# Kernel tuning notes

Hardware: AMD Instinct MI355X
Metric: run time of the kernel (lower is better)

The kernel has to match this reference:

```python
import jax, jax.numpy as jnp
import numpy as np

DECAY = 0.99
EPS = 1e-05


def setup_inputs() -> dict:
    key = jax.random.key(0)
    k1, k2, k3, k4 = jax.random.split(key, 4)
    x = jax.random.normal(k1, (32, 64, 64, 64), jnp.float32)          # [B,H,W,dim]
    embed = jax.random.normal(k2, (64, 1024), jnp.float32)            # [dim, n_embed] buffer
    cluster_size = jax.random.uniform(k3, (1024,), jnp.float32)       # EMA cluster-size buffer
    embed_avg = jax.random.normal(k4, (64, 1024), jnp.float32)        # EMA embed-avg buffer
    return {"x": x, "embed": embed, "cluster_size": cluster_size, "embed_avg": embed_avg}


def reference(x, embed, cluster_size, embed_avg):
    dim = x.shape[-1]
    n_embed = embed.shape[1]
    flatten = x.reshape(-1, dim)                                      # [N, dim]
    # squared distances: ||f||^2 - 2 f.E + ||e||^2   -> [N, n_embed]
    dist = ((flatten * flatten).sum(1, keepdims=True)
            - 2.0 * (flatten @ embed)
            + (embed * embed).sum(0, keepdims=True))
    idx = jnp.argmin(dist, axis=1)                                    # [N]
    quantize = jnp.take(embed.T, idx, axis=0).reshape(x.shape)        # codebook gather
    embed_ind = idx.reshape(x.shape[:-1])

    # EMA codebook update (training branch); stats detached as in torch (buffers, .data ops)
    fl = jax.lax.stop_gradient(flatten)
    onehot_sum = jax.ops.segment_sum(jnp.ones_like(idx, dtype=x.dtype), idx, num_segments=n_embed)
    embed_sum = jax.ops.segment_sum(fl, idx, num_segments=n_embed).T  # [dim, n_embed]
    new_cluster_size = DECAY * cluster_size + (1.0 - DECAY) * onehot_sum
    new_embed_avg = DECAY * embed_avg + (1.0 - DECAY) * embed_sum
    n = new_cluster_size.sum()
    cs = (new_cluster_size + EPS) / (n + n_embed * EPS) * n
    new_embed = new_embed_avg / cs[None, :]

    diff = jnp.mean((jax.lax.stop_gradient(quantize) - x) ** 2)       # commitment loss
    quantize_st = x + jax.lax.stop_gradient(quantize - x)             # straight-through
    return (quantize_st, diff, embed_ind, new_cluster_size, new_embed_avg, new_embed)
```

## Files before the change

### kernel.cpp

```cpp
#include <hip/hip_runtime.h>


#define N_ROWS 131072
#define DIM    64
#define NEMB   1024
#define FLAG_CAP 131072
#define TAU 0.02f
#define NRANGE 32

static constexpr float DECAYF = 0.99f;
static constexpr float OMDF   = (float)(1.0 - 0.99);
static constexpr float EPSF   = 1e-5f;
static constexpr float NEPSF  = (float)(1024 * 1e-5);

typedef __attribute__((ext_vector_type(8))) short short8;
typedef __attribute__((ext_vector_type(4))) float f32x4;

static __device__ __forceinline__ unsigned short f2bf(float f) {
    unsigned int u = __builtin_bit_cast(unsigned int, f);
    unsigned int r = (u + 0x7FFFu + ((u >> 16) & 1u)) >> 16;
    return (unsigned short)r;
}
static __device__ __forceinline__ float bf2f(unsigned short h) {
    unsigned int u = ((unsigned int)h) << 16;
    return __builtin_bit_cast(float, u);
}

#define WS_ESUM    0
#define WS_CNTF    65536
#define WS_DIFF    66560
#define WS_FLAGCNT 66561
#define WS_N       66562
#define WS_EE      66564
#define WS_EMBEDT  67588
#define WS_IDX     133124
#define WS_FLAGLST 264196
#define WS_BFRAG   395268
#define WS_CNTPART 460804
#define WS_PART    493572
#define WS_NEED_BYTES ((size_t)(WS_PART + NRANGE * 65536) * 4)

__global__ void prep_kernel(const float* __restrict__ embed,
                            float* __restrict__ embedT,
                            float* __restrict__ ee,
                            uint4* __restrict__ BfragG) {
    int tid = blockIdx.x * 256 + threadIdx.x;
    for (int i = 0; i < 4; ++i) {
        int id = i * 16384 + tid;
        int d = id >> 10, e = id & 1023;
        embedT[e * 64 + d] = embed[id];
    }
    if (tid < NEMB) {
        float s = 0.f;
        for (int d = 0; d < DIM; ++d) {
            float v = embed[d * 1024 + tid];
            s = fmaf(v, v, s);
        }
        ee[tid] = s;
    }
    int fid  = tid >> 6;
    int lane = tid & 63;
    int hl = fid & 1, kt = (fid >> 1) & 1, ct = fid >> 2;
    int col = ct * 16 + (lane & 15);
    int k0  = kt * 32 + (lane >> 4) * 8;
    unsigned short u[8];
    #pragma unroll
    for (int j = 0; j < 8; ++j) {
        float v = -2.0f * embed[(k0 + j) * 1024 + col];
        unsigned short h = f2bf(v);
        if (hl) h = f2bf(v - bf2f(h));
        u[j] = h;
    }
    uint4 wv;
    wv.x = (unsigned)u[0] | ((unsigned)u[1] << 16);
    wv.y = (unsigned)u[2] | ((unsigned)u[3] << 16);
    wv.z = (unsigned)u[4] | ((unsigned)u[5] << 16);
    wv.w = (unsigned)u[6] | ((unsigned)u[7] << 16);
    BfragG[fid * 64 + lane] = wv;
}

__global__ __launch_bounds__(256) void dist_kernel(
        const float* __restrict__ x, const uint4* __restrict__ BfragG,
        const float* __restrict__ ee, const float* __restrict__ embedT,
        float* __restrict__ out_q, float* __restrict__ out_ind,
        int* __restrict__ ws_idx, float* __restrict__ ws_diff,
        int* __restrict__ ws_flagcnt, int* __restrict__ ws_flaglist) {
    __shared__ float sEE[1024];
    __shared__ int   sIdx[128];
    __shared__ float red[4];

    const int t = threadIdx.x;
    const int w = t >> 6, lane = t & 63;
    const int quad = lane >> 4, wl = lane & 15;
    const int rbase = blockIdx.x * 128;

    short8 a_hi[2][2], a_lo[2][2];
    #pragma unroll
    for (int rt = 0; rt < 2; ++rt) {
        int row = rbase + w * 32 + rt * 16 + wl;
        #pragma unroll
        for (int kt = 0; kt < 2; ++kt) {
            const float* px = x + (size_t)row * 64 + kt * 32 + quad * 8;
            float4 v0 = *(const float4*)px;
            float4 v1 = *(const float4*)(px + 4);
            float vv[8] = {v0.x, v0.y, v0.z, v0.w, v1.x, v1.y, v1.z, v1.w};
            short8 ah, al;
            #pragma unroll
            for (int j = 0; j < 8; ++j) {
                unsigned short h = f2bf(vv[j]);
                ah[j] = (short)h;
                al[j] = (short)f2bf(vv[j] - bf2f(h));
            }
            a_hi[rt][kt] = ah; a_lo[rt][kt] = al;
        }
    }

    for (int i = t; i < 1024; i += 256) sEE[i] = ee[i];

    float b1[8], b2[8];
    int   i1[8];
    #pragma unroll
    for (int s = 0; s < 8; ++s) { b1[s] = 3.4e38f; b2[s] = 3.4e38f; i1[s] = 0; }

    const f32x4 zacc = {0.f, 0.f, 0.f, 0.f};

    __syncthreads();

    const uint4* bg = BfragG + lane;
    uint4 nb0 = bg[0], nb1 = bg[64], nb2 = bg[128], nb3 = bg[192];
    for (int g = 0; g < 64; ++g) {
        uint4 c_b0 = nb0, c_b1 = nb1, c_b2 = nb2, c_b3 = nb3;
        if (g < 63) {
            const uint4* p = bg + (g + 1) * 256;
            nb0 = p[0]; nb1 = p[64]; nb2 = p[128]; nb3 = p[192];
        }
        short8 bh0 = __builtin_bit_cast(short8, c_b0);
        short8 bl0 = __builtin_bit_cast(short8, c_b1);
        short8 bh1 = __builtin_bit_cast(short8, c_b2);
        short8 bl1 = __builtin_bit_cast(short8, c_b3);
        int col = g * 16 + wl;
        float eec = sEE[col];
        #pragma unroll
        for (int rt = 0; rt < 2; ++rt) {
            f32x4 c0 = __builtin_amdgcn_mfma_f32_16x16x32_bf16(a_lo[rt][0], bh0, zacc, 0, 0, 0);
            f32x4 c1 = __builtin_amdgcn_mfma_f32_16x16x32_bf16(a_lo[rt][1], bh1, zacc, 0, 0, 0);
            c0 = __builtin_amdgcn_mfma_f32_16x16x32_bf16(a_hi[rt][0], bl0, c0, 0, 0, 0);
            c1 = __builtin_amdgcn_mfma_f32_16x16x32_bf16(a_hi[rt][1], bl1, c1, 0, 0, 0);
            c0 = __builtin_amdgcn_mfma_f32_16x16x32_bf16(a_hi[rt][0], bh0, c0, 0, 0, 0);
            c1 = __builtin_amdgcn_mfma_f32_16x16x32_bf16(a_hi[rt][1], bh1, c1, 0, 0, 0);
            #pragma unroll
            for (int reg = 0; reg < 4; ++reg) {
                float s = c0[reg] + c1[reg] + eec;
                int st = rt * 4 + reg;
                bool lt = s < b1[st];
                b2[st] = fminf(fmaxf(s, b1[st]), b2[st]);
                i1[st] = lt ? col : i1[st];
                b1[st] = fminf(s, b1[st]);
            }
        }
    }

    for (int m = 1; m < 16; m <<= 1) {
        #pragma unroll
        for (int s = 0; s < 8; ++s) {
            float ob1 = __shfl_xor(b1[s], m);
            int   oi1 = __shfl_xor(i1[s], m);
            float ob2 = __shfl_xor(b2[s], m);
            if (ob1 < b1[s] || (ob1 == b1[s] && oi1 < i1[s])) {
                b2[s] = fminf(b1[s], ob2); b1[s] = ob1; i1[s] = oi1;
            } else {
                b2[s] = fminf(b2[s], ob1);
            }
        }
    }
    if (wl == 0) {
        #pragma unroll
        for (int s = 0; s < 8; ++s) {
            int rt = s >> 2, reg = s & 3;
            int rloc = w * 32 + rt * 16 + quad * 4 + reg;
            int row = rbase + rloc;
            sIdx[rloc] = i1[s];
            ws_idx[row] = i1[s];
            out_ind[row] = (float)i1[s];
            if (b2[s] - b1[s] < TAU) {
                int pos = atomicAdd(ws_flagcnt, 1);
                if (pos < FLAG_CAP) ws_flaglist[pos] = row;
            }
        }
    }
    __syncthreads();

    {
        int r = t >> 1, hh = t & 1;
        int e = sIdx[r];
        const float4* et = (const float4*)(embedT + e * 64 + hh * 32);
        const float4* xr = (const float4*)(x + (size_t)(rbase + r) * 64 + hh * 32);
        float4*       qo = (float4*)(out_q + (size_t)(rbase + r) * 64 + hh * 32);
        float dsum = 0.f;
        #pragma unroll
        for (int v = 0; v < 8; ++v) {
            float4 q4 = et[v];
            float4 x4 = xr[v];
            float dx = q4.x - x4.x, dy = q4.y - x4.y, dz = q4.z - x4.z, dw = q4.w - x4.w;
            float4 o;
            o.x = x4.x + dx; o.y = x4.y + dy; o.z = x4.z + dz; o.w = x4.w + dw;
            qo[v] = o;
            dsum += dx * dx + dy * dy + dz * dz + dw * dw;
        }
        for (int o2 = 32; o2 > 0; o2 >>= 1) dsum += __shfl_down(dsum, o2);
        if (lane == 0) red[w] = dsum;
        __syncthreads();
        if (t == 0) atomicAdd(ws_diff, red[0] + red[1] + red[2] + red[3]);
    }
}

__global__ __launch_bounds__(256) void recheck_kernel(
        const float* __restrict__ x, const float* __restrict__ embed,
        const float* __restrict__ embedT, const float* __restrict__ ee,
        const int* __restrict__ flagcnt, const int* __restrict__ flaglist,
        int* __restrict__ ws_idx, float* __restrict__ out_ind,
        float* __restrict__ out_q, float* __restrict__ ws_diff) {
    __shared__ float sx[8][64];
    __shared__ float sff[8];
    __shared__ int   srow[8];
    __shared__ float sbd[8][256];
    __shared__ int   sbi[8][256];
    const int t = threadIdx.x;
    const int w = t >> 6, lane = t & 63;
    int cnt = *flagcnt;
    if (cnt > FLAG_CAP) cnt = FLAG_CAP;
    int ntiles = (cnt + 7) >> 3;
    for (int tile = blockIdx.x; tile < ntiles; tile += gridDim.x) {
        int base = tile * 8;
        int nr = cnt - base; if (nr > 8) nr = 8;
        __syncthreads();
        if (t < nr) srow[t] = flaglist[base + t];
        __syncthreads();
        for (int l = t; l < nr * 64; l += 256)
            sx[l >> 6][l & 63] = x[(size_t)srow[l >> 6] * 64 + (l & 63)];
        __syncthreads();
        if (t < nr) {
            float ff = 0.f;
            for (int k = 0; k < 64; ++k) ff = fmaf(sx[t][k], sx[t][k], ff);
            sff[t] = ff;
        }
        float acc[8][4];
        #pragma unroll
        for (int r = 0; r < 8; ++r)
            #pragma unroll
            for (int j = 0; j < 4; ++j) acc[r][j] = 0.f;
        int c0 = t * 4;
        for (int k = 0; k < 64; ++k) {
            float4 e4 = *(const float4*)(embed + k * 1024 + c0);
            #pragma unroll
            for (int r = 0; r < 8; ++r) {
                float xk = sx[r][k];
                acc[r][0] = fmaf(xk, e4.x, acc[r][0]);
                acc[r][1] = fmaf(xk, e4.y, acc[r][1]);
                acc[r][2] = fmaf(xk, e4.z, acc[r][2]);
                acc[r][3] = fmaf(xk, e4.w, acc[r][3]);
            }
        }
        __syncthreads();
        #pragma unroll
        for (int r = 0; r < 8; ++r) {
            float ff = sff[r];
            float bd = 3.4e38f; int bi = 0;
            #pragma unroll
            for (int j = 0; j < 4; ++j) {
                float d = (ff - 2.f * acc[r][j]) + ee[c0 + j];
                if (d < bd) { bd = d; bi = c0 + j; }
            }
            sbd[r][t] = bd; sbi[r][t] = bi;
        }
        __syncthreads();
        #pragma unroll
        for (int rr = 0; rr < 2; ++rr) {
            int r = w * 2 + rr;
            if (r < nr) {
                float bd = sbd[r][lane]; int bi = sbi[r][lane];
                #pragma unroll
                for (int k2 = 1; k2 < 4; ++k2) {
                    float od = sbd[r][lane + 64 * k2];
                    int   oi = sbi[r][lane + 64 * k2];
                    if (od < bd || (od == bd && oi < bi)) { bd = od; bi = oi; }
                }
                for (int m = 32; m > 0; m >>= 1) {
                    float od = __shfl_xor(bd, m);
                    int   oi = __shfl_xor(bi, m);
                    if (od < bd || (od == bd && oi < bi)) { bd = od; bi = oi; }
                }
                int row = srow[r];
                int oi_old = ws_idx[row];
                if (bi != oi_old) {
                    float xv = sx[r][lane];
                    float dn   = embedT[bi * 64 + lane] - xv;
                    float dold = embedT[oi_old * 64 + lane] - xv;
                    out_q[(size_t)row * 64 + lane] = xv + dn;
                    float delta = dn * dn - dold * dold;
                    for (int o = 32; o > 0; o >>= 1) delta += __shfl_down(delta, o);
                    if (lane == 0) {
                        ws_idx[row] = bi;
                        out_ind[row] = (float)bi;
                        atomicAdd(ws_diff, delta);
                    }
                }
            }
        }
    }
}

__global__ __launch_bounds__(512) void scatter_kernel(
        const int* __restrict__ idx, const float* __restrict__ x,
        float* __restrict__ part_or_esum, float* __restrict__ cntp_or_cntf,
        int use_atomic) {
    __shared__ float shist[8192];
    __shared__ float scnt[1024];
    const int t = threadIdx.x;
    const int rb = blockIdx.x >> 3, oct = blockIdx.x & 7;
    const int w = t >> 6, lane = t & 63;
    const int g = lane >> 3, d = lane & 7;

    for (int i = t; i < 8192; i += 512) shist[i] = 0.f;
    if (oct == 0) for (int i = t; i < 1024; i += 512) scnt[i] = 0.f;
    __syncthreads();

    const int row0 = rb * 4096 + w * 512;
    int rcur = row0 + g;
    int e_n = idx[rcur];
    float x_n = x[(size_t)rcur * 64 + oct * 8 + d];
    for (int it = 0; it < 64; ++it) {
        int e = e_n; float xv = x_n;
        int rnext = rcur + 8;
        if (it < 63) {
            e_n = idx[rnext];
            x_n = x[(size_t)rnext * 64 + oct * 8 + d];
        }
        rcur = rnext;
        atomicAdd(&shist[e * 8 + d], xv);
        if (oct == 0 && d == 0) atomicAdd(&scnt[e], 1.0f);
    }
    __syncthreads();

    if (!use_atomic) {
        float* dst = part_or_esum + (size_t)blockIdx.x * 8192;
        for (int out = t; out < 8192; out += 512)
            dst[out] = shist[(out & 1023) * 8 + (out >> 10)];
        if (oct == 0) {
            float* cdst = cntp_or_cntf + rb * 1024;
            for (int i = t; i < 1024; i += 512) cdst[i] = scnt[i];
        }
    } else {
        for (int out = t; out < 8192; out += 512) {
            float v = shist[(out & 1023) * 8 + (out >> 10)];
            if (v != 0.f)
                atomicAdd(&part_or_esum[(oct * 8 + (out >> 10)) * 1024 + (out & 1023)], v);
        }
        if (oct == 0) {
            for (int i = t; i < 1024; i += 512) {
                float c = scnt[i];
                if (c != 0.f) atomicAdd(&cntp_or_cntf[i], c);
            }
        }
    }
}

__global__ __launch_bounds__(1024) void finalize1(
        const float* __restrict__ cluster_size, const float* __restrict__ cntp,
        int nrb, const float* __restrict__ ws_diff, float* __restrict__ out_diff,
        float* __restrict__ out_ncs, float* __restrict__ ws_n) {
    int t = threadIdx.x;
    float c = 0.f;
    for (int k = 0; k < nrb; ++k) c += cntp[k * 1024 + t];
    float ncs = DECAYF * cluster_size[t] + OMDF * c;
    out_ncs[t] = ncs;
    __shared__ float sred[16];
    float v = ncs;
    for (int o = 32; o > 0; o >>= 1) v += __shfl_down(v, o);
    if ((t & 63) == 0) sred[t >> 6] = v;
    __syncthreads();
    if (t == 0) {
        float n = 0.f;
        for (int i = 0; i < 16; ++i) n += sred[i];
        ws_n[0] = n;
        out_diff[0] = ws_diff[0] * (1.0f / 8388608.0f);
    }
}

__global__ __launch_bounds__(256) void finalize2(
        const float* __restrict__ embed_avg, const float* __restrict__ part,
        int nrb, const float* __restrict__ out_ncs, const float* __restrict__ ws_n,
        float* __restrict__ out_nea, float* __restrict__ out_ne) {
    int j = blockIdx.x * 256 + threadIdx.x;
    float es = 0.f;
    for (int k = 0; k < nrb; ++k) es += part[(size_t)k * 65536 + j];
    float n = ws_n[0];
    float nea = DECAYF * embed_avg[j] + OMDF * es;
    out_nea[j] = nea;
    float ncs = out_ncs[j & 1023];
    float cs = (ncs + EPSF) / (n + NEPSF) * n;
    out_ne[j] = nea / cs;
}

extern "C" void kernel_launch(void* const* d_in, const int* in_sizes, int n_in,
                              void* d_out, int out_size, void* d_ws, size_t ws_size,
                              hipStream_t stream) {
    const float* x            = (const float*)d_in[0];
    const float* embed        = (const float*)d_in[1];
    const float* cluster_size = (const float*)d_in[2];
    const float* embed_avg    = (const float*)d_in[3];

    float* out = (float*)d_out;
    float* out_q    = out;
    float* out_diff = out + 8388608;
    float* out_ind  = out + 8388609;
    float* out_ncs  = out + 8519681;
    float* out_nea  = out + 8520705;
    float* out_ne   = out + 8586241;

    float* ws = (float*)d_ws;
    float* ws_esum     = ws + WS_ESUM;
    float* ws_cntf     = ws + WS_CNTF;
    float* ws_diff     = ws + WS_DIFF;
    int*   ws_flagcnt  = (int*)(ws + WS_FLAGCNT);
    float* ws_n        = ws + WS_N;
    float* ws_ee       = ws + WS_EE;
    float* ws_embedT   = ws + WS_EMBEDT;
    int*   ws_idx      = (int*)(ws + WS_IDX);
    int*   ws_flaglist = (int*)(ws + WS_FLAGLST);
    uint4* ws_Bfrag    = (uint4*)(ws + WS_BFRAG);
    float* ws_cntpart  = ws + WS_CNTPART;
    float* ws_part     = ws + WS_PART;

    const int use_part = (ws_size >= WS_NEED_BYTES) ? 1 : 0;

    if (use_part) {
        hipMemsetAsync(ws + WS_DIFF, 0, 8, stream);
    } else {
        hipMemsetAsync(d_ws, 0, (size_t)(WS_FLAGCNT + 1) * 4, stream);
    }

    prep_kernel<<<64, 256, 0, stream>>>(embed, ws_embedT, ws_ee, ws_Bfrag);
    dist_kernel<<<N_ROWS / 128, 256, 0, stream>>>(x, ws_Bfrag, ws_ee, ws_embedT,
                                                  out_q, out_ind, ws_idx, ws_diff,
                                                  ws_flagcnt, ws_flaglist);
    recheck_kernel<<<512, 256, 0, stream>>>(x, embed, ws_embedT, ws_ee,
                                            ws_flagcnt, ws_flaglist,
                                            ws_idx, out_ind, out_q, ws_diff);
    scatter_kernel<<<NRANGE * 8, 512, 0, stream>>>(
        ws_idx, x,
        use_part ? ws_part : ws_esum,
        use_part ? ws_cntpart : ws_cntf,
        use_part ? 0 : 1);
    finalize1<<<1, 1024, 0, stream>>>(cluster_size,
                                      use_part ? ws_cntpart : ws_cntf,
                                      use_part ? NRANGE : 1,
                                      ws_diff, out_diff, out_ncs, ws_n);
    finalize2<<<256, 256, 0, stream>>>(embed_avg,
                                       use_part ? ws_part : ws_esum,
                                       use_part ? NRANGE : 1,
                                       out_ncs, ws_n, out_nea, out_ne);
}
```

Baseline: 269.5 us.

## Halve rows per dist block, widen scatter blocks, double recheck grid

The distance kernel now processes 64 rows per block, with one 16-row tile per wave instead of two. This cuts register use and doubles the block count, but each codebook fragment load is reused across half as many rows. The scatter kernel moves to 1024-thread blocks, each thread doing half the iterations, and its block index is remapped. The recheck grid is doubled to spread the flagged-row work across more blocks.

```diff
diff --git a/kernel.cpp b/kernel.cpp
--- a/kernel.cpp
+++ b/kernel.cpp
@@ -86,18 +86,17 @@
         int* __restrict__ ws_idx, float* __restrict__ ws_diff,
         int* __restrict__ ws_flagcnt, int* __restrict__ ws_flaglist) {
     __shared__ float sEE[1024];
-    __shared__ int   sIdx[128];
+    __shared__ int   sIdx[64];
     __shared__ float red[4];
 
     const int t = threadIdx.x;
     const int w = t >> 6, lane = t & 63;
     const int quad = lane >> 4, wl = lane & 15;
-    const int rbase = blockIdx.x * 128;
-
-    short8 a_hi[2][2], a_lo[2][2];
-    #pragma unroll
-    for (int rt = 0; rt < 2; ++rt) {
-        int row = rbase + w * 32 + rt * 16 + wl;
+    const int rbase = blockIdx.x * 64;
+
+    short8 a_hi[2], a_lo[2];
+    {
+        int row = rbase + w * 16 + wl;
         #pragma unroll
         for (int kt = 0; kt < 2; ++kt) {
             const float* px = x + (size_t)row * 64 + kt * 32 + quad * 8;
@@ -111,16 +110,16 @@
                 ah[j] = (short)h;
                 al[j] = (short)f2bf(vv[j] - bf2f(h));
             }
-            a_hi[rt][kt] = ah; a_lo[rt][kt] = al;
+            a_hi[kt] = ah; a_lo[kt] = al;
         }
     }
 
     for (int i = t; i < 1024; i += 256) sEE[i] = ee[i];
 
-    float b1[8], b2[8];
-    int   i1[8];
+    float b1[4], b2[4];
+    int   i1[4];
     #pragma unroll
-    for (int s = 0; s < 8; ++s) { b1[s] = 3.4e38f; b2[s] = 3.4e38f; i1[s] = 0; }
+    for (int s = 0; s < 4; ++s) { b1[s] = 3.4e38f; b2[s] = 3.4e38f; i1[s] = 0; }
 
     const f32x4 zacc = {0.f, 0.f, 0.f, 0.f};
 
@@ -140,29 +139,27 @@
         short8 bl1 = __builtin_bit_cast(short8, c_b3);
         int col = g * 16 + wl;
         float eec = sEE[col];
-        #pragma unroll
-        for (int rt = 0; rt < 2; ++rt) {
-            f32x4 c0 = __builtin_amdgcn_mfma_f32_16x16x32_bf16(a_lo[rt][0], bh0, zacc, 0, 0, 0);
-            f32x4 c1 = __builtin_amdgcn_mfma_f32_16x16x32_bf16(a_lo[rt][1], bh1, zacc, 0, 0, 0);
-            c0 = __builtin_amdgcn_mfma_f32_16x16x32_bf16(a_hi[rt][0], bl0, c0, 0, 0, 0);
-            c1 = __builtin_amdgcn_mfma_f32_16x16x32_bf16(a_hi[rt][1], bl1, c1, 0, 0, 0);
-            c0 = __builtin_amdgcn_mfma_f32_16x16x32_bf16(a_hi[rt][0], bh0, c0, 0, 0, 0);
-            c1 = __builtin_amdgcn_mfma_f32_16x16x32_bf16(a_hi[rt][1], bh1, c1, 0, 0, 0);
+        {
+            f32x4 c0 = __builtin_amdgcn_mfma_f32_16x16x32_bf16(a_lo[0], bh0, zacc, 0, 0, 0);
+            f32x4 c1 = __builtin_amdgcn_mfma_f32_16x16x32_bf16(a_lo[1], bh1, zacc, 0, 0, 0);
+            c0 = __builtin_amdgcn_mfma_f32_16x16x32_bf16(a_hi[0], bl0, c0, 0, 0, 0);
+            c1 = __builtin_amdgcn_mfma_f32_16x16x32_bf16(a_hi[1], bl1, c1, 0, 0, 0);
+            c0 = __builtin_amdgcn_mfma_f32_16x16x32_bf16(a_hi[0], bh0, c0, 0, 0, 0);
+            c1 = __builtin_amdgcn_mfma_f32_16x16x32_bf16(a_hi[1], bh1, c1, 0, 0, 0);
             #pragma unroll
             for (int reg = 0; reg < 4; ++reg) {
                 float s = c0[reg] + c1[reg] + eec;
-                int st = rt * 4 + reg;
-                bool lt = s < b1[st];
-                b2[st] = fminf(fmaxf(s, b1[st]), b2[st]);
-                i1[st] = lt ? col : i1[st];
-                b1[st] = fminf(s, b1[st]);
+                bool lt = s < b1[reg];
+                b2[reg] = fminf(fmaxf(s, b1[reg]), b2[reg]);
+                i1[reg] = lt ? col : i1[reg];
+                b1[reg] = fminf(s, b1[reg]);
             }
         }
     }
 
     for (int m = 1; m < 16; m <<= 1) {
         #pragma unroll
-        for (int s = 0; s < 8; ++s) {
+        for (int s = 0; s < 4; ++s) {
             float ob1 = __shfl_xor(b1[s], m);
             int   oi1 = __shfl_xor(i1[s], m);
             float ob2 = __shfl_xor(b2[s], m);
@@ -175,9 +172,8 @@
     }
     if (wl == 0) {
         #pragma unroll
-        for (int s = 0; s < 8; ++s) {
-            int rt = s >> 2, reg = s & 3;
-            int rloc = w * 32 + rt * 16 + quad * 4 + reg;
+        for (int s = 0; s < 4; ++s) {
+            int rloc = w * 16 + quad * 4 + s;
             int row = rbase + rloc;
             sIdx[rloc] = i1[s];
             ws_idx[row] = i1[s];
@@ -191,14 +187,14 @@
     __syncthreads();
 
     {
-        int r = t >> 1, hh = t & 1;
+        int r = t >> 2, hh = t & 3;
         int e = sIdx[r];
-        const float4* et = (const float4*)(embedT + e * 64 + hh * 32);
-        const float4* xr = (const float4*)(x + (size_t)(rbase + r) * 64 + hh * 32);
-        float4*       qo = (float4*)(out_q + (size_t)(rbase + r) * 64 + hh * 32);
+        const float4* et = (const float4*)(embedT + e * 64 + hh * 16);
+        const float4* xr = (const float4*)(x + (size_t)(rbase + r) * 64 + hh * 16);
+        float4*       qo = (float4*)(out_q + (size_t)(rbase + r) * 64 + hh * 16);
         float dsum = 0.f;
         #pragma unroll
-        for (int v = 0; v < 8; ++v) {
+        for (int v = 0; v < 4; ++v) {
             float4 q4 = et[v];
             float4 x4 = xr[v];
             float dx = q4.x - x4.x, dy = q4.y - x4.y, dz = q4.z - x4.z, dw = q4.w - x4.w;
@@ -310,29 +306,32 @@
     }
 }
 
-__global__ __launch_bounds__(512) void scatter_kernel(
+__global__ __launch_bounds__(1024) void scatter_kernel(
         const int* __restrict__ idx, const float* __restrict__ x,
         float* __restrict__ part_or_esum, float* __restrict__ cntp_or_cntf,
         int use_atomic) {
     __shared__ float shist[8192];
     __shared__ float scnt[1024];
     const int t = threadIdx.x;
-    const int rb = blockIdx.x >> 3, oct = blockIdx.x & 7;
+    const int bid = blockIdx.x;
+    const int oct = (bid >> 3) & 7;
+    const int rb  = (bid & 7) | ((bid >> 6) << 3);
+    const int sid = rb * 8 + oct;
     const int w = t >> 6, lane = t & 63;
     const int g = lane >> 3, d = lane & 7;
 
-    for (int i = t; i < 8192; i += 512) shist[i] = 0.f;
-    if (oct == 0) for (int i = t; i < 1024; i += 512) scnt[i] = 0.f;
+    for (int i = t; i < 8192; i += 1024) shist[i] = 0.f;
+    if (oct == 0) { if (t < 1024) scnt[t] = 0.f; }
     __syncthreads();
 
-    const int row0 = rb * 4096 + w * 512;
+    const int row0 = rb * 4096 + w * 256;
     int rcur = row0 + g;
     int e_n = idx[rcur];
     float x_n = x[(size_t)rcur * 64 + oct * 8 + d];
-    for (int it = 0; it < 64; ++it) {
+    for (int it = 0; it < 32; ++it) {
         int e = e_n; float xv = x_n;
         int rnext = rcur + 8;
-        if (it < 63) {
+        if (it < 31) {
             e_n = idx[rnext];
             x_n = x[(size_t)rnext * 64 + oct * 8 + d];
         }
@@ -343,23 +342,23 @@
     __syncthreads();
 
     if (!use_atomic) {
-        float* dst = part_or_esum + (size_t)blockIdx.x * 8192;
-        for (int out = t; out < 8192; out += 512)
+        float* dst = part_or_esum + (size_t)sid * 8192;
+        for (int out = t; out < 8192; out += 1024)
             dst[out] = shist[(out & 1023) * 8 + (out >> 10)];
         if (oct == 0) {
             float* cdst = cntp_or_cntf + rb * 1024;
-            for (int i = t; i < 1024; i += 512) cdst[i] = scnt[i];
+            if (t < 1024) cdst[t] = scnt[t];
         }
     } else {
-        for (int out = t; out < 8192; out += 512) {
+        for (int out = t; out < 8192; out += 1024) {
             float v = shist[(out & 1023) * 8 + (out >> 10)];
             if (v != 0.f)
                 atomicAdd(&part_or_esum[(oct * 8 + (out >> 10)) * 1024 + (out & 1023)], v);
         }
         if (oct == 0) {
-            for (int i = t; i < 1024; i += 512) {
-                float c = scnt[i];
-                if (c != 0.f) atomicAdd(&cntp_or_cntf[i], c);
+            if (t < 1024) {
+                float c = scnt[t];
+                if (c != 0.f) atomicAdd(&cntp_or_cntf[t], c);
             }
         }
     }
@@ -441,13 +440,13 @@
     }
 
     prep_kernel<<<64, 256, 0, stream>>>(embed, ws_embedT, ws_ee, ws_Bfrag);
-    dist_kernel<<<N_ROWS / 128, 256, 0, stream>>>(x, ws_Bfrag, ws_ee, ws_embedT,
-                                                  out_q, out_ind, ws_idx, ws_diff,
-                                                  ws_flagcnt, ws_flaglist);
-    recheck_kernel<<<512, 256, 0, stream>>>(x, embed, ws_embedT, ws_ee,
-                                            ws_flagcnt, ws_flaglist,
-                                            ws_idx, out_ind, out_q, ws_diff);
-    scatter_kernel<<<NRANGE * 8, 512, 0, stream>>>(
+    dist_kernel<<<N_ROWS / 64, 256, 0, stream>>>(x, ws_Bfrag, ws_ee, ws_embedT,
+                                                 out_q, out_ind, ws_idx, ws_diff,
+                                                 ws_flagcnt, ws_flaglist);
+    recheck_kernel<<<1024, 256, 0, stream>>>(x, embed, ws_embedT, ws_ee,
+                                             ws_flagcnt, ws_flaglist,
+                                             ws_idx, out_ind, out_q, ws_diff);
+    scatter_kernel<<<NRANGE * 8, 1024, 0, stream>>>(
         ws_idx, x,
         use_part ? ws_part : ws_esum,
         use_part ? ws_cntpart : ws_cntf,
```

Result: slower. 305.3 us (+13.3%).
